# Optimization experiments

Measured on AMD Instinct MI355X. Metric: run time of the kernel, lower is better.

Reference implementation:

```python
import jax, jax.numpy as jnp
import numpy as np

NUM_EMBEDDINGS = 512
EMBEDDING_DIM = 64
COMMITMENT_COST = 0.25


def setup_inputs() -> dict:
    key = jax.random.key(0)
    kx, kc = jax.random.split(key)
    x = jax.random.normal(kx, (32, 64, 64, EMBEDDING_DIM), dtype=jnp.float32)
    # nn.Embedding weight initialized uniform(-1/K, 1/K)
    codebook = jax.random.uniform(
        kc, (NUM_EMBEDDINGS, EMBEDDING_DIM), dtype=jnp.float32,
        minval=-1.0 / NUM_EMBEDDINGS, maxval=1.0 / NUM_EMBEDDINGS)
    return {"x": x, "codebook": codebook}


def reference(x, codebook):
    D = codebook.shape[1]
    flat = x.reshape(-1, D)  # [N, D]
    # squared euclidean distances; argmin is identical to cdist(p=2) argmin
    d2 = (jnp.sum(flat * flat, axis=-1, keepdims=True)
          - 2.0 * (flat @ codebook.T)
          + jnp.sum(codebook * codebook, axis=-1))  # [N, K]
    idx = jnp.argmin(d2, axis=1)  # [N]
    quantized = codebook[idx].reshape(x.shape)  # gather == one-hot @ codebook
    e_latent_loss = jnp.mean((jax.lax.stop_gradient(quantized) - x) ** 2)
    q_latent_loss = jnp.mean((quantized - jax.lax.stop_gradient(x)) ** 2)
    loss = q_latent_loss + COMMITMENT_COST * e_latent_loss
    # straight-through estimator
    quantized_st = x + jax.lax.stop_gradient(quantized - x)
    return quantized_st, loss
```

## Files before the change

### kernel.cpp

```cpp
#include <hip/hip_runtime.h>

#define DIMS 64
#define KCB 512
#define OUT_Q 8388608
#define MAIN_WGS 512

typedef float f32x4 __attribute__((ext_vector_type(4)));
typedef float f4    __attribute__((ext_vector_type(4)));
typedef short short8 __attribute__((ext_vector_type(8)));


static __device__ __forceinline__ unsigned int f2bf(float f) {
    unsigned int u = __float_as_uint(f);
    unsigned int r = u + 0x7FFFu + ((u >> 16) & 1u);
    return r >> 16;
}

__global__ void vq_prep(const float* __restrict__ cb, float* __restrict__ ws) {
    int t = blockIdx.x * blockDim.x + threadIdx.x;
    if (t < 4096) {
        int kt = t >> 7, rest = t & 127;
        int h = rest >> 6, l = rest & 63;
        int row = kt * 16 + (l & 15);
        int col = h * 32 + ((l >> 4) & 3) * 8;
        const f4* p = (const f4*)(cb + row * DIMS + col);
        f4 u0 = p[0], u1 = p[1];
        unsigned int* dst = (unsigned int*)((char*)ws + 4096 + kt * 2048 + h * 1024 + l * 16);
        dst[0] = (f2bf(u0[1]) << 16) | f2bf(u0[0]);
        dst[1] = (f2bf(u0[3]) << 16) | f2bf(u0[2]);
        dst[2] = (f2bf(u1[1]) << 16) | f2bf(u1[0]);
        dst[3] = (f2bf(u1[3]) << 16) | f2bf(u1[2]);
    } else if (t < 4096 + KCB) {
        int r = t - 4096;
        const f4* p = (const f4*)(cb + r * DIMS);
        float s = 0.0f;
#pragma unroll
        for (int i = 0; i < DIMS / 4; ++i) {
            f4 v = p[i];
            s += v[0]*v[0] + v[1]*v[1] + v[2]*v[2] + v[3]*v[3];
        }
        ws[512 + r] = -0.5f * s;
    }
}

__global__ __launch_bounds__(512, 4) void vq_main(const float* __restrict__ x,
                                                  const float* __restrict__ cb,
                                                  float* __restrict__ out,
                                                  float* __restrict__ ws) {
    __shared__ f4 lds_b4[4096];

    const int tid  = threadIdx.x;
    const int lane = tid & 63;
    const int wid  = tid >> 6;
    const int wave = blockIdx.x * 8 + wid;
    const long rowbase = (long)wave * 32;
    const int r15 = lane & 15;
    const int g   = lane >> 4;

    {
        const f4* src = (const f4*)((const char*)ws + 4096);
#pragma unroll
        for (int r = 0; r < 8; ++r)
            lds_b4[r * 512 + tid] = src[r * 512 + tid];
    }

    const float* nbase = ws + 512;
    float n0 = nbase[lane], n1 = nbase[64 + lane], n2 = nbase[128 + lane],
          n3 = nbase[192 + lane], n4 = nbase[256 + lane], n5 = nbase[320 + lane],
          n6 = nbase[384 + lane], n7 = nbase[448 + lane];

    short8 A00, A01, A10, A11;
    {
        const float* xa = x + (rowbase + r15) * DIMS + g * 8;
#define LOADA(FR, OFF)                                                         \
        {                                                                      \
            const f4* p_ = (const f4*)(xa + (OFF));                            \
            f4 a_ = p_[0], b_ = p_[1];                                         \
            union { unsigned int u[4]; short8 s; } q_;                         \
            asm("v_cvt_pk_bf16_f32 %0, %1, %2" : "=v"(q_.u[0]) : "v"(a_[0]), "v"(a_[1])); \
            asm("v_cvt_pk_bf16_f32 %0, %1, %2" : "=v"(q_.u[1]) : "v"(a_[2]), "v"(a_[3])); \
            asm("v_cvt_pk_bf16_f32 %0, %1, %2" : "=v"(q_.u[2]) : "v"(b_[0]), "v"(b_[1])); \
            asm("v_cvt_pk_bf16_f32 %0, %1, %2" : "=v"(q_.u[3]) : "v"(b_[2]), "v"(b_[3])); \
            FR = q_.s;                                                         \
        }
        LOADA(A00, 0)
        LOADA(A01, 32)
        LOADA(A10, 16 * DIMS)
        LOADA(A11, 16 * DIMS + 32)
#undef LOADA
    }

    __syncthreads();

    float bv00 = -3.4e38f, bv01 = -3.4e38f, bv02 = -3.4e38f, bv03 = -3.4e38f;
    float bv10 = -3.4e38f, bv11 = -3.4e38f, bv12 = -3.4e38f, bv13 = -3.4e38f;

    const char* ldsb = (const char*)lds_b4;
    const int laneoff = lane * 16;

#define NSEL(KT) ((KT>>2)==0?n0:(KT>>2)==1?n1:(KT>>2)==2?n2:(KT>>2)==3?n3: \
                  (KT>>2)==4?n4:(KT>>2)==5?n5:(KT>>2)==6?n6:n7)
#define PKMAX(BV, S)                                                           \
    BV = fmaxf(BV, __uint_as_float((__float_as_uint(S) & 0xFFFFFE00u) | kr));

#pragma unroll
    for (int kt = 0; kt < 32; ++kt) {
        short8 b0 = *(const short8*)(ldsb + kt * 2048 + laneoff);
        short8 b1 = *(const short8*)(ldsb + kt * 2048 + 1024 + laneoff);
        float ic = __shfl(NSEL(kt), ((kt & 3) << 4) + r15, 64);
        f32x4 init = {ic, ic, ic, ic};
        f32x4 a0 = __builtin_amdgcn_mfma_f32_16x16x32_bf16(A00, b0, init, 0, 0, 0);
        a0       = __builtin_amdgcn_mfma_f32_16x16x32_bf16(A01, b1, a0,  0, 0, 0);
        f32x4 a1 = __builtin_amdgcn_mfma_f32_16x16x32_bf16(A10, b0, init, 0, 0, 0);
        a1       = __builtin_amdgcn_mfma_f32_16x16x32_bf16(A11, b1, a1,  0, 0, 0);
        const unsigned int kr = (unsigned int)(kt * 16 + r15);
        PKMAX(bv00, a0[0]) PKMAX(bv01, a0[1]) PKMAX(bv02, a0[2]) PKMAX(bv03, a0[3])
        PKMAX(bv10, a1[0]) PKMAX(bv11, a1[1]) PKMAX(bv12, a1[2]) PKMAX(bv13, a1[3])
    }
#undef PKMAX
#undef NSEL

#pragma unroll
    for (int st = 0; st < 4; ++st) {
        const int m = 1 << st;
        bv00 = fmaxf(bv00, __shfl_xor(bv00, m, 64));
        bv01 = fmaxf(bv01, __shfl_xor(bv01, m, 64));
        bv02 = fmaxf(bv02, __shfl_xor(bv02, m, 64));
        bv03 = fmaxf(bv03, __shfl_xor(bv03, m, 64));
        bv10 = fmaxf(bv10, __shfl_xor(bv10, m, 64));
        bv11 = fmaxf(bv11, __shfl_xor(bv11, m, 64));
        bv12 = fmaxf(bv12, __shfl_xor(bv12, m, 64));
        bv13 = fmaxf(bv13, __shfl_xor(bv13, m, 64));
    }

    const int orow = lane >> 2;
    const int cseg = lane & 3;
    const int j2   = orow & 3;
    int idx0 = (int)(__float_as_uint(j2 == 0 ? bv00 : j2 == 1 ? bv01 : j2 == 2 ? bv02 : bv03) & 511u);
    int idx1 = (int)(__float_as_uint(j2 == 0 ? bv10 : j2 == 1 ? bv11 : j2 == 2 ? bv12 : bv13) & 511u);

    float lsum = 0.0f;
#define EPI(IDX, TOFF)                                                     \
    {                                                                      \
        const long row_ = rowbase + (TOFF) + orow;                         \
        const f4* cq_ = (const f4*)(cb + (long)(IDX) * DIMS + cseg * 16);  \
        const f4* xr_ = (const f4*)(x + row_ * DIMS + cseg * 16);          \
        f4* op_      = (f4*)(out + row_ * DIMS + cseg * 16);               \
        _Pragma("unroll")                                                  \
        for (int u = 0; u < 4; ++u) {                                      \
            f4 q_ = cq_[u];                                                \
            f4 xv_ = xr_[u];                                               \
            op_[u] = q_;                                                   \
            f4 d_ = q_ - xv_;                                              \
            lsum += d_[0]*d_[0] + d_[1]*d_[1] + d_[2]*d_[2] + d_[3]*d_[3]; \
        }                                                                  \
    }
    EPI(idx0, 0)
    EPI(idx1, 16)
#undef EPI

#pragma unroll
    for (int s = 0; s < 6; ++s) lsum += __shfl_xor(lsum, 1 << s, 64);
    __syncthreads();
    float* lsred = (float*)lds_b4;
    if (lane == 0) lsred[wid] = lsum;
    __syncthreads();
    if (tid == 0) {
        ws[blockIdx.x] = lsred[0] + lsred[1] + lsred[2] + lsred[3]
                       + lsred[4] + lsred[5] + lsred[6] + lsred[7];
    }
}

__global__ __launch_bounds__(256) void vq_final(const float* __restrict__ ws,
                                                float* __restrict__ out) {
    const int t = threadIdx.x;
    float s = ws[t] + ws[t + 256];
#pragma unroll
    for (int st = 0; st < 6; ++st) s += __shfl_xor(s, 1 << st, 64);
    __shared__ float w2[4];
    if ((t & 63) == 0) w2[t >> 6] = s;
    __syncthreads();
    if (t == 0) {
        float total = w2[0] + w2[1] + w2[2] + w2[3];
        out[OUT_Q] = 1.25f * total / 8388608.0f;
    }
}

extern "C" void kernel_launch(void* const* d_in, const int* in_sizes, int n_in,
                              void* d_out, int out_size, void* d_ws, size_t ws_size,
                              hipStream_t stream) {
    const float* x  = (const float*)d_in[0];
    const float* cb = (const float*)d_in[1];
    float* out = (float*)d_out;
    float* ws  = (float*)d_ws;
    vq_prep<<<18, 256, 0, stream>>>(cb, ws);
    vq_main<<<MAIN_WGS, 512, 0, stream>>>(x, cb, out, ws);
    vq_final<<<1, 256, 0, stream>>>(ws, out);
}
```

Before: 34.21 us.

## Compute loss from argmin scores and move codebook norms to LDS

Drops the epilogue re-read of x for the loss. The loss is now rebuilt algebraically as ||x||^2 minus twice the packed best score, with ||x||^2 accumulated during the A-fragment load. It also moves the per-code -0.5||c||^2 bias from eight per-lane registers plus a shuffle to an LDS array read inside the MFMA loop. This saves memory traffic in the epilogue, but the loss now comes from bf16 MFMA dot products with 9 bits of the score mantissa masked off, so accuracy may suffer. LDS grows slightly.

```diff
diff --git a/kernel.cpp b/kernel.cpp
--- a/kernel.cpp
+++ b/kernel.cpp
@@ -47,7 +47,7 @@
                                                   const float* __restrict__ cb,
                                                   float* __restrict__ out,
                                                   float* __restrict__ ws) {
-    __shared__ f4 lds_b4[4096];
+    __shared__ char lds[66560];
 
     const int tid  = threadIdx.x;
     const int lane = tid & 63;
@@ -59,23 +59,23 @@
 
     {
         const f4* src = (const f4*)((const char*)ws + 4096);
+        f4* ldsv = (f4*)lds;
 #pragma unroll
         for (int r = 0; r < 8; ++r)
-            lds_b4[r * 512 + tid] = src[r * 512 + tid];
-    }
-
-    const float* nbase = ws + 512;
-    float n0 = nbase[lane], n1 = nbase[64 + lane], n2 = nbase[128 + lane],
-          n3 = nbase[192 + lane], n4 = nbase[256 + lane], n5 = nbase[320 + lane],
-          n6 = nbase[384 + lane], n7 = nbase[448 + lane];
+            ldsv[r * 512 + tid] = src[r * 512 + tid];
+        ((float*)(lds + 65536))[tid] = ws[512 + tid];
+    }
 
     short8 A00, A01, A10, A11;
+    float xn0 = 0.0f, xn1 = 0.0f;
     {
         const float* xa = x + (rowbase + r15) * DIMS + g * 8;
-#define LOADA(FR, OFF)                                                         \
+#define LOADA(FR, OFF, XN)                                                     \
         {                                                                      \
             const f4* p_ = (const f4*)(xa + (OFF));                            \
             f4 a_ = p_[0], b_ = p_[1];                                         \
+            XN += a_[0]*a_[0] + a_[1]*a_[1] + a_[2]*a_[2] + a_[3]*a_[3]        \
+                + b_[0]*b_[0] + b_[1]*b_[1] + b_[2]*b_[2] + b_[3]*b_[3];       \
             union { unsigned int u[4]; short8 s; } q_;                         \
             asm("v_cvt_pk_bf16_f32 %0, %1, %2" : "=v"(q_.u[0]) : "v"(a_[0]), "v"(a_[1])); \
             asm("v_cvt_pk_bf16_f32 %0, %1, %2" : "=v"(q_.u[1]) : "v"(a_[2]), "v"(a_[3])); \
@@ -83,23 +83,24 @@
             asm("v_cvt_pk_bf16_f32 %0, %1, %2" : "=v"(q_.u[3]) : "v"(b_[2]), "v"(b_[3])); \
             FR = q_.s;                                                         \
         }
-        LOADA(A00, 0)
-        LOADA(A01, 32)
-        LOADA(A10, 16 * DIMS)
-        LOADA(A11, 16 * DIMS + 32)
+        LOADA(A00, 0, xn0)
+        LOADA(A01, 32, xn0)
+        LOADA(A10, 16 * DIMS, xn1)
+        LOADA(A11, 16 * DIMS + 32, xn1)
 #undef LOADA
     }
+    xn0 += __shfl_xor(xn0, 16, 64);  xn0 += __shfl_xor(xn0, 32, 64);
+    xn1 += __shfl_xor(xn1, 16, 64);  xn1 += __shfl_xor(xn1, 32, 64);
 
     __syncthreads();
 
     float bv00 = -3.4e38f, bv01 = -3.4e38f, bv02 = -3.4e38f, bv03 = -3.4e38f;
     float bv10 = -3.4e38f, bv11 = -3.4e38f, bv12 = -3.4e38f, bv13 = -3.4e38f;
 
-    const char* ldsb = (const char*)lds_b4;
+    const char*  ldsb = lds;
+    const float* ldsn = (const float*)(lds + 65536);
     const int laneoff = lane * 16;
 
-#define NSEL(KT) ((KT>>2)==0?n0:(KT>>2)==1?n1:(KT>>2)==2?n2:(KT>>2)==3?n3: \
-                  (KT>>2)==4?n4:(KT>>2)==5?n5:(KT>>2)==6?n6:n7)
 #define PKMAX(BV, S)                                                           \
     BV = fmaxf(BV, __uint_as_float((__float_as_uint(S) & 0xFFFFFE00u) | kr));
 
@@ -107,7 +108,7 @@
     for (int kt = 0; kt < 32; ++kt) {
         short8 b0 = *(const short8*)(ldsb + kt * 2048 + laneoff);
         short8 b1 = *(const short8*)(ldsb + kt * 2048 + 1024 + laneoff);
-        float ic = __shfl(NSEL(kt), ((kt & 3) << 4) + r15, 64);
+        float ic = ldsn[kt * 16 + r15];
         f32x4 init = {ic, ic, ic, ic};
         f32x4 a0 = __builtin_amdgcn_mfma_f32_16x16x32_bf16(A00, b0, init, 0, 0, 0);
         a0       = __builtin_amdgcn_mfma_f32_16x16x32_bf16(A01, b1, a0,  0, 0, 0);
@@ -118,7 +119,6 @@
         PKMAX(bv10, a1[0]) PKMAX(bv11, a1[1]) PKMAX(bv12, a1[2]) PKMAX(bv13, a1[3])
     }
 #undef PKMAX
-#undef NSEL
 
 #pragma unroll
     for (int st = 0; st < 4; ++st) {
@@ -139,30 +139,32 @@
     int idx0 = (int)(__float_as_uint(j2 == 0 ? bv00 : j2 == 1 ? bv01 : j2 == 2 ? bv02 : bv03) & 511u);
     int idx1 = (int)(__float_as_uint(j2 == 0 ? bv10 : j2 == 1 ? bv11 : j2 == 2 ? bv12 : bv13) & 511u);
 
-    float lsum = 0.0f;
 #define EPI(IDX, TOFF)                                                     \
     {                                                                      \
         const long row_ = rowbase + (TOFF) + orow;                         \
         const f4* cq_ = (const f4*)(cb + (long)(IDX) * DIMS + cseg * 16);  \
-        const f4* xr_ = (const f4*)(x + row_ * DIMS + cseg * 16);          \
         f4* op_      = (f4*)(out + row_ * DIMS + cseg * 16);               \
         _Pragma("unroll")                                                  \
-        for (int u = 0; u < 4; ++u) {                                      \
-            f4 q_ = cq_[u];                                                \
-            f4 xv_ = xr_[u];                                               \
-            op_[u] = q_;                                                   \
-            f4 d_ = q_ - xv_;                                              \
-            lsum += d_[0]*d_[0] + d_[1]*d_[1] + d_[2]*d_[2] + d_[3]*d_[3]; \
-        }                                                                  \
+        for (int u = 0; u < 4; ++u) op_[u] = cq_[u];                       \
     }
     EPI(idx0, 0)
     EPI(idx1, 16)
 #undef EPI
 
+    float lsum = 0.0f;
+    if (g == (r15 >> 2)) {
+        const int jp = r15 & 3;
+        float s0 = jp == 0 ? bv00 : jp == 1 ? bv01 : jp == 2 ? bv02 : bv03;
+        float s1 = jp == 0 ? bv10 : jp == 1 ? bv11 : jp == 2 ? bv12 : bv13;
+        s0 = __uint_as_float(__float_as_uint(s0) & 0xFFFFFE00u);
+        s1 = __uint_as_float(__float_as_uint(s1) & 0xFFFFFE00u);
+        lsum = (xn0 - 2.0f * s0) + (xn1 - 2.0f * s1);
+    }
 #pragma unroll
     for (int s = 0; s < 6; ++s) lsum += __shfl_xor(lsum, 1 << s, 64);
-    __syncthreads();
-    float* lsred = (float*)lds_b4;
+
+    __syncthreads();
+    float* lsred = (float*)lds;
     if (lane == 0) lsred[wid] = lsum;
     __syncthreads();
     if (tid == 0) {
```

After: 31.53 us. 1.08x faster.

## Split codebook across waves, drop prep kernel, compute loss from distances

Applied to the files above, without the earlier changes.

Removes the codebook preprocessing kernel. Each wave now loads and converts its own 64-entry slice of the codebook straight into registers and computes those entries' norms, then scores all 128 rows of the workgroup against that slice. The argmax is combined across the eight waves through LDS. The loss is taken algebraically as the squared x norm minus twice the best score, so x is no longer re-read in the epilogue. Twice as many workgroups are launched. The trade-off is that the loss now depends on bf16 MFMA scores rather than an exact fp32 difference, and there is an extra LDS reduction stage.

```diff
diff --git a/kernel.cpp b/kernel.cpp
--- a/kernel.cpp
+++ b/kernel.cpp
@@ -1,180 +1,178 @@
 #include <hip/hip_runtime.h>
 
 #define DIMS 64
-#define KCB 512
 #define OUT_Q 8388608
-#define MAIN_WGS 512
+#define MAIN_WGS 1024
 
 typedef float f32x4 __attribute__((ext_vector_type(4)));
 typedef float f4    __attribute__((ext_vector_type(4)));
 typedef short short8 __attribute__((ext_vector_type(8)));
 
+union U8 { unsigned int u[4]; short8 s; };
 
-static __device__ __forceinline__ unsigned int f2bf(float f) {
-    unsigned int u = __float_as_uint(f);
-    unsigned int r = u + 0x7FFFu + ((u >> 16) & 1u);
-    return r >> 16;
-}
 
-__global__ void vq_prep(const float* __restrict__ cb, float* __restrict__ ws) {
-    int t = blockIdx.x * blockDim.x + threadIdx.x;
-    if (t < 4096) {
-        int kt = t >> 7, rest = t & 127;
-        int h = rest >> 6, l = rest & 63;
-        int row = kt * 16 + (l & 15);
-        int col = h * 32 + ((l >> 4) & 3) * 8;
-        const f4* p = (const f4*)(cb + row * DIMS + col);
-        f4 u0 = p[0], u1 = p[1];
-        unsigned int* dst = (unsigned int*)((char*)ws + 4096 + kt * 2048 + h * 1024 + l * 16);
-        dst[0] = (f2bf(u0[1]) << 16) | f2bf(u0[0]);
-        dst[1] = (f2bf(u0[3]) << 16) | f2bf(u0[2]);
-        dst[2] = (f2bf(u1[1]) << 16) | f2bf(u1[0]);
-        dst[3] = (f2bf(u1[3]) << 16) | f2bf(u1[2]);
-    } else if (t < 4096 + KCB) {
-        int r = t - 4096;
-        const f4* p = (const f4*)(cb + r * DIMS);
-        float s = 0.0f;
-#pragma unroll
-        for (int i = 0; i < DIMS / 4; ++i) {
-            f4 v = p[i];
-            s += v[0]*v[0] + v[1]*v[1] + v[2]*v[2] + v[3]*v[3];
-        }
-        ws[512 + r] = -0.5f * s;
-    }
-}
+#define CVT8(Q, A, B)                                                          \
+    asm("v_cvt_pk_bf16_f32 %0, %1, %2" : "=v"(Q.u[0]) : "v"(A[0]), "v"(A[1])); \
+    asm("v_cvt_pk_bf16_f32 %0, %1, %2" : "=v"(Q.u[1]) : "v"(A[2]), "v"(A[3])); \
+    asm("v_cvt_pk_bf16_f32 %0, %1, %2" : "=v"(Q.u[2]) : "v"(B[0]), "v"(B[1])); \
+    asm("v_cvt_pk_bf16_f32 %0, %1, %2" : "=v"(Q.u[3]) : "v"(B[2]), "v"(B[3]));
 
 __global__ __launch_bounds__(512, 4) void vq_main(const float* __restrict__ x,
                                                   const float* __restrict__ cb,
                                                   float* __restrict__ out,
                                                   float* __restrict__ ws) {
-    __shared__ f4 lds_b4[4096];
+    __shared__ float lds_best[8 * 128];
+    __shared__ float lds_xn[128];
+    __shared__ int   lds_idx[128];
+    __shared__ float lds_part[2];
 
     const int tid  = threadIdx.x;
     const int lane = tid & 63;
     const int wid  = tid >> 6;
-    const int wave = blockIdx.x * 8 + wid;
-    const long rowbase = (long)wave * 32;
-    const int r15 = lane & 15;
-    const int g   = lane >> 4;
+    const int r15  = lane & 15;
+    const int g    = lane >> 4;
+    const long wgrow = (long)blockIdx.x * 128;
+
+    short8 B00, B01, B10, B11, B20, B21, B30, B31;
+    float ic0, ic1, ic2, ic3;
+#define LOADB(KK, B0, B1, IC) {                                                \
+        const float* crow_ = cb + (((wid << 2) + KK) * 16 + r15) * DIMS + (g << 3); \
+        f4 a_ = *(const f4*)crow_;                                             \
+        f4 b_ = *(const f4*)(crow_ + 4);                                       \
+        f4 c_ = *(const f4*)(crow_ + 32);                                      \
+        f4 d_ = *(const f4*)(crow_ + 36);                                      \
+        U8 q_; CVT8(q_, a_, b_) B0 = q_.s; CVT8(q_, c_, d_) B1 = q_.s;         \
+        float nn_ = a_[0]*a_[0]+a_[1]*a_[1]+a_[2]*a_[2]+a_[3]*a_[3]            \
+                  + b_[0]*b_[0]+b_[1]*b_[1]+b_[2]*b_[2]+b_[3]*b_[3]            \
+                  + c_[0]*c_[0]+c_[1]*c_[1]+c_[2]*c_[2]+c_[3]*c_[3]            \
+                  + d_[0]*d_[0]+d_[1]*d_[1]+d_[2]*d_[2]+d_[3]*d_[3];           \
+        nn_ += __shfl_xor(nn_, 16, 64);  nn_ += __shfl_xor(nn_, 32, 64);       \
+        IC = -0.5f * nn_; }
+    LOADB(0, B00, B01, ic0)
+    LOADB(1, B10, B11, ic1)
+    LOADB(2, B20, B21, ic2)
+    LOADB(3, B30, B31, ic3)
+#undef LOADB
+
+    float bv00=-3.4e38f, bv01=-3.4e38f, bv02=-3.4e38f, bv03=-3.4e38f;
+    float bv10=-3.4e38f, bv11=-3.4e38f, bv12=-3.4e38f, bv13=-3.4e38f;
+    float bv20=-3.4e38f, bv21=-3.4e38f, bv22=-3.4e38f, bv23=-3.4e38f;
+    float bv30=-3.4e38f, bv31=-3.4e38f, bv32=-3.4e38f, bv33=-3.4e38f;
+    float bv40=-3.4e38f, bv41=-3.4e38f, bv42=-3.4e38f, bv43=-3.4e38f;
+    float bv50=-3.4e38f, bv51=-3.4e38f, bv52=-3.4e38f, bv53=-3.4e38f;
+    float bv60=-3.4e38f, bv61=-3.4e38f, bv62=-3.4e38f, bv63=-3.4e38f;
+    float bv70=-3.4e38f, bv71=-3.4e38f, bv72=-3.4e38f, bv73=-3.4e38f;
+    float xn0, xn1, xn2, xn3, xn4, xn5, xn6, xn7;
+
+#define KSTEP(KK, B0, B1, IC, BV0, BV1, BV2, BV3) {                            \
+        f32x4 init_ = {IC, IC, IC, IC};                                        \
+        f32x4 acc_ = __builtin_amdgcn_mfma_f32_16x16x32_bf16(A0_, B0, init_, 0, 0, 0); \
+        acc_       = __builtin_amdgcn_mfma_f32_16x16x32_bf16(A1_, B1, acc_, 0, 0, 0);  \
+        const unsigned int kr_ = (unsigned int)((((wid << 2) + KK) << 4) + r15); \
+        BV0 = fmaxf(BV0, __uint_as_float((__float_as_uint(acc_[0]) & 0xFFFFFE00u) | kr_)); \
+        BV1 = fmaxf(BV1, __uint_as_float((__float_as_uint(acc_[1]) & 0xFFFFFE00u) | kr_)); \
+        BV2 = fmaxf(BV2, __uint_as_float((__float_as_uint(acc_[2]) & 0xFFFFFE00u) | kr_)); \
+        BV3 = fmaxf(BV3, __uint_as_float((__float_as_uint(acc_[3]) & 0xFFFFFE00u) | kr_)); }
+
+#define TILE(T, BV0, BV1, BV2, BV3, XN) {                                      \
+        const float* xa_ = x + (wgrow + T * 16 + r15) * DIMS + (g << 3);       \
+        f4 a_ = *(const f4*)xa_;                                               \
+        f4 b_ = *(const f4*)(xa_ + 4);                                         \
+        f4 c_ = *(const f4*)(xa_ + 32);                                        \
+        f4 d_ = *(const f4*)(xa_ + 36);                                        \
+        float xp_ = a_[0]*a_[0]+a_[1]*a_[1]+a_[2]*a_[2]+a_[3]*a_[3]            \
+                  + b_[0]*b_[0]+b_[1]*b_[1]+b_[2]*b_[2]+b_[3]*b_[3]            \
+                  + c_[0]*c_[0]+c_[1]*c_[1]+c_[2]*c_[2]+c_[3]*c_[3]            \
+                  + d_[0]*d_[0]+d_[1]*d_[1]+d_[2]*d_[2]+d_[3]*d_[3];           \
+        xp_ += __shfl_xor(xp_, 16, 64);  xp_ += __shfl_xor(xp_, 32, 64);       \
+        XN = xp_;                                                              \
+        U8 q_; short8 A0_, A1_;                                                \
+        CVT8(q_, a_, b_) A0_ = q_.s;                                           \
+        CVT8(q_, c_, d_) A1_ = q_.s;                                           \
+        KSTEP(0, B00, B01, ic0, BV0, BV1, BV2, BV3)                            \
+        KSTEP(1, B10, B11, ic1, BV0, BV1, BV2, BV3)                            \
+        KSTEP(2, B20, B21, ic2, BV0, BV1, BV2, BV3)                            \
+        KSTEP(3, B30, B31, ic3, BV0, BV1, BV2, BV3) }
+
+    TILE(0, bv00, bv01, bv02, bv03, xn0)
+    TILE(1, bv10, bv11, bv12, bv13, xn1)
+    TILE(2, bv20, bv21, bv22, bv23, xn2)
+    TILE(3, bv30, bv31, bv32, bv33, xn3)
+    TILE(4, bv40, bv41, bv42, bv43, xn4)
+    TILE(5, bv50, bv51, bv52, bv53, xn5)
+    TILE(6, bv60, bv61, bv62, bv63, xn6)
+    TILE(7, bv70, bv71, bv72, bv73, xn7)
+#undef TILE
+#undef KSTEP
+
+#define RED(BV) { BV = fmaxf(BV, __shfl_xor(BV, 1, 64));                       \
+                  BV = fmaxf(BV, __shfl_xor(BV, 2, 64));                       \
+                  BV = fmaxf(BV, __shfl_xor(BV, 4, 64));                       \
+                  BV = fmaxf(BV, __shfl_xor(BV, 8, 64)); }
+    RED(bv00) RED(bv01) RED(bv02) RED(bv03)
+    RED(bv10) RED(bv11) RED(bv12) RED(bv13)
+    RED(bv20) RED(bv21) RED(bv22) RED(bv23)
+    RED(bv30) RED(bv31) RED(bv32) RED(bv33)
+    RED(bv40) RED(bv41) RED(bv42) RED(bv43)
+    RED(bv50) RED(bv51) RED(bv52) RED(bv53)
+    RED(bv60) RED(bv61) RED(bv62) RED(bv63)
+    RED(bv70) RED(bv71) RED(bv72) RED(bv73)
+#undef RED
+
+    if (r15 == 0) {
+#define ST(T, BV0, BV1, BV2, BV3) {                                            \
+        const int rb_ = T * 16 + (g << 2);                                     \
+        lds_best[wid * 128 + rb_]     = BV0;                                   \
+        lds_best[wid * 128 + rb_ + 1] = BV1;                                   \
+        lds_best[wid * 128 + rb_ + 2] = BV2;                                   \
+        lds_best[wid * 128 + rb_ + 3] = BV3; }
+        ST(0, bv00, bv01, bv02, bv03)
+        ST(1, bv10, bv11, bv12, bv13)
+        ST(2, bv20, bv21, bv22, bv23)
+        ST(3, bv30, bv31, bv32, bv33)
+        ST(4, bv40, bv41, bv42, bv43)
+        ST(5, bv50, bv51, bv52, bv53)
+        ST(6, bv60, bv61, bv62, bv63)
+        ST(7, bv70, bv71, bv72, bv73)
+#undef ST
+    }
+    if (tid < 16) {
+        lds_xn[tid]       = xn0;  lds_xn[16 + tid]  = xn1;
+        lds_xn[32 + tid]  = xn2;  lds_xn[48 + tid]  = xn3;
+        lds_xn[64 + tid]  = xn4;  lds_xn[80 + tid]  = xn5;
+        lds_xn[96 + tid]  = xn6;  lds_xn[112 + tid] = xn7;
+    }
+    __syncthreads();
+
+    float lred = 0.0f;
+    if (tid < 128) {
+        float m = lds_best[tid];
+#pragma unroll
+        for (int w = 1; w < 8; ++w) m = fmaxf(m, lds_best[w * 128 + tid]);
+        const unsigned int mb = __float_as_uint(m);
+        lds_idx[tid] = (int)(mb & 511u);
+        lred = lds_xn[tid] - 2.0f * __uint_as_float(mb & 0xFFFFFE00u);
+    }
+#pragma unroll
+    for (int s = 0; s < 6; ++s) lred += __shfl_xor(lred, 1 << s, 64);
+    if (tid == 0)  lds_part[0] = lred;
+    if (tid == 64) lds_part[1] = lred;
+    __syncthreads();
 
     {
-        const f4* src = (const f4*)((const char*)ws + 4096);
-#pragma unroll
-        for (int r = 0; r < 8; ++r)
-            lds_b4[r * 512 + tid] = src[r * 512 + tid];
+        const int erow = tid >> 2, eseg = tid & 3;
+        const long eidx = (long)lds_idx[erow];
+        const f4* cq = (const f4*)(cb + eidx * DIMS + eseg * 16);
+        f4* op = (f4*)(out + (wgrow + erow) * DIMS + eseg * 16);
+        op[0] = cq[0]; op[1] = cq[1]; op[2] = cq[2]; op[3] = cq[3];
     }
-
-    const float* nbase = ws + 512;
-    float n0 = nbase[lane], n1 = nbase[64 + lane], n2 = nbase[128 + lane],
-          n3 = nbase[192 + lane], n4 = nbase[256 + lane], n5 = nbase[320 + lane],
-          n6 = nbase[384 + lane], n7 = nbase[448 + lane];
-
-    short8 A00, A01, A10, A11;
-    {
-        const float* xa = x + (rowbase + r15) * DIMS + g * 8;
-#define LOADA(FR, OFF)                                                         \
-        {                                                                      \
-            const f4* p_ = (const f4*)(xa + (OFF));                            \
-            f4 a_ = p_[0], b_ = p_[1];                                         \
-            union { unsigned int u[4]; short8 s; } q_;                         \
-            asm("v_cvt_pk_bf16_f32 %0, %1, %2" : "=v"(q_.u[0]) : "v"(a_[0]), "v"(a_[1])); \
-            asm("v_cvt_pk_bf16_f32 %0, %1, %2" : "=v"(q_.u[1]) : "v"(a_[2]), "v"(a_[3])); \
-            asm("v_cvt_pk_bf16_f32 %0, %1, %2" : "=v"(q_.u[2]) : "v"(b_[0]), "v"(b_[1])); \
-            asm("v_cvt_pk_bf16_f32 %0, %1, %2" : "=v"(q_.u[3]) : "v"(b_[2]), "v"(b_[3])); \
-            FR = q_.s;                                                         \
-        }
-        LOADA(A00, 0)
-        LOADA(A01, 32)
-        LOADA(A10, 16 * DIMS)
-        LOADA(A11, 16 * DIMS + 32)
-#undef LOADA
-    }
-
-    __syncthreads();
-
-    float bv00 = -3.4e38f, bv01 = -3.4e38f, bv02 = -3.4e38f, bv03 = -3.4e38f;
-    float bv10 = -3.4e38f, bv11 = -3.4e38f, bv12 = -3.4e38f, bv13 = -3.4e38f;
-
-    const char* ldsb = (const char*)lds_b4;
-    const int laneoff = lane * 16;
-
-#define NSEL(KT) ((KT>>2)==0?n0:(KT>>2)==1?n1:(KT>>2)==2?n2:(KT>>2)==3?n3: \
-                  (KT>>2)==4?n4:(KT>>2)==5?n5:(KT>>2)==6?n6:n7)
-#define PKMAX(BV, S)                                                           \
-    BV = fmaxf(BV, __uint_as_float((__float_as_uint(S) & 0xFFFFFE00u) | kr));
-
-#pragma unroll
-    for (int kt = 0; kt < 32; ++kt) {
-        short8 b0 = *(const short8*)(ldsb + kt * 2048 + laneoff);
-        short8 b1 = *(const short8*)(ldsb + kt * 2048 + 1024 + laneoff);
-        float ic = __shfl(NSEL(kt), ((kt & 3) << 4) + r15, 64);
-        f32x4 init = {ic, ic, ic, ic};
-        f32x4 a0 = __builtin_amdgcn_mfma_f32_16x16x32_bf16(A00, b0, init, 0, 0, 0);
-        a0       = __builtin_amdgcn_mfma_f32_16x16x32_bf16(A01, b1, a0,  0, 0, 0);
-        f32x4 a1 = __builtin_amdgcn_mfma_f32_16x16x32_bf16(A10, b0, init, 0, 0, 0);
-        a1       = __builtin_amdgcn_mfma_f32_16x16x32_bf16(A11, b1, a1,  0, 0, 0);
-        const unsigned int kr = (unsigned int)(kt * 16 + r15);
-        PKMAX(bv00, a0[0]) PKMAX(bv01, a0[1]) PKMAX(bv02, a0[2]) PKMAX(bv03, a0[3])
-        PKMAX(bv10, a1[0]) PKMAX(bv11, a1[1]) PKMAX(bv12, a1[2]) PKMAX(bv13, a1[3])
-    }
-#undef PKMAX
-#undef NSEL
-
-#pragma unroll
-    for (int st = 0; st < 4; ++st) {
-        const int m = 1 << st;
-        bv00 = fmaxf(bv00, __shfl_xor(bv00, m, 64));
-        bv01 = fmaxf(bv01, __shfl_xor(bv01, m, 64));
-        bv02 = fmaxf(bv02, __shfl_xor(bv02, m, 64));
-        bv03 = fmaxf(bv03, __shfl_xor(bv03, m, 64));
-        bv10 = fmaxf(bv10, __shfl_xor(bv10, m, 64));
-        bv11 = fmaxf(bv11, __shfl_xor(bv11, m, 64));
-        bv12 = fmaxf(bv12, __shfl_xor(bv12, m, 64));
-        bv13 = fmaxf(bv13, __shfl_xor(bv13, m, 64));
-    }
-
-    const int orow = lane >> 2;
-    const int cseg = lane & 3;
-    const int j2   = orow & 3;
-    int idx0 = (int)(__float_as_uint(j2 == 0 ? bv00 : j2 == 1 ? bv01 : j2 == 2 ? bv02 : bv03) & 511u);
-    int idx1 = (int)(__float_as_uint(j2 == 0 ? bv10 : j2 == 1 ? bv11 : j2 == 2 ? bv12 : bv13) & 511u);
-
-    float lsum = 0.0f;
-#define EPI(IDX, TOFF)                                                     \
-    {                                                                      \
-        const long row_ = rowbase + (TOFF) + orow;                         \
-        const f4* cq_ = (const f4*)(cb + (long)(IDX) * DIMS + cseg * 16);  \
-        const f4* xr_ = (const f4*)(x + row_ * DIMS + cseg * 16);          \
-        f4* op_      = (f4*)(out + row_ * DIMS + cseg * 16);               \
-        _Pragma("unroll")                                                  \
-        for (int u = 0; u < 4; ++u) {                                      \
-            f4 q_ = cq_[u];                                                \
-            f4 xv_ = xr_[u];                                               \
-            op_[u] = q_;                                                   \
-            f4 d_ = q_ - xv_;                                              \
-            lsum += d_[0]*d_[0] + d_[1]*d_[1] + d_[2]*d_[2] + d_[3]*d_[3]; \
-        }                                                                  \
-    }
-    EPI(idx0, 0)
-    EPI(idx1, 16)
-#undef EPI
-
-#pragma unroll
-    for (int s = 0; s < 6; ++s) lsum += __shfl_xor(lsum, 1 << s, 64);
-    __syncthreads();
-    float* lsred = (float*)lds_b4;
-    if (lane == 0) lsred[wid] = lsum;
-    __syncthreads();
-    if (tid == 0) {
-        ws[blockIdx.x] = lsred[0] + lsred[1] + lsred[2] + lsred[3]
-                       + lsred[4] + lsred[5] + lsred[6] + lsred[7];
-    }
+    if (tid == 0) ws[blockIdx.x] = lds_part[0] + lds_part[1];
 }
 
 __global__ __launch_bounds__(256) void vq_final(const float* __restrict__ ws,
                                                 float* __restrict__ out) {
     const int t = threadIdx.x;
-    float s = ws[t] + ws[t + 256];
+    float s = ws[t] + ws[t + 256] + ws[t + 512] + ws[t + 768];
 #pragma unroll
     for (int st = 0; st < 6; ++st) s += __shfl_xor(s, 1 << st, 64);
     __shared__ float w2[4];
@@ -193,7 +191,6 @@
     const float* cb = (const float*)d_in[1];
     float* out = (float*)d_out;
     float* ws  = (float*)d_ws;
-    vq_prep<<<18, 256, 0, stream>>>(cb, ws);
     vq_main<<<MAIN_WGS, 512, 0, stream>>>(x, cb, out, ws);
     vq_final<<<1, 256, 0, stream>>>(ws, out);
 }
```

Result: slower. 62.99 us (+84.1%).
